# Kernel tuning notes

Hardware: AMD Instinct MI355X
Metric: run time of the kernel (lower is better)

Reference implementation:

```python
import jax, jax.numpy as jnp
import numpy as np

B, A, D, H, S, C, NB = 8192, 8, 4096, 1024, 32, 32, 8
BS = D // NB          # 512: hidden block size
IBS = (2 * H) // NB   # 256: input block size (gru input = action_embed ++ stoch_embed)
UNIMIX = 0.01


def setup_inputs() -> dict:
    key = jax.random.key(0)
    ks = jax.random.split(key, 16)
    rn = lambda k, shape, s=1.0: jax.random.normal(k, shape, jnp.float32) * s
    return {
        'deterministic': rn(ks[0], (B, D)),
        'stochastic': jax.random.uniform(ks[1], (B, S, C), jnp.float32),
        'prev_action': rn(ks[2], (B, A)),
        'embed': rn(ks[3], (B, H)),
        'is_first': jax.random.bernoulli(ks[4], 0.1, (B,)),
        # encoders (nn.Linear stores weight as [out, in])
        'W_act': rn(ks[5], (H, A), 1.0 / np.sqrt(A)), 'b_act': jnp.zeros((H,)),
        'W_stoch': rn(ks[6], (H, S * C), 1.0 / np.sqrt(S * C)), 'b_stoch': jnp.zeros((H,)),
        # block-diagonal GRU: per-block [3*BS, IBS] and [3*BS, BS]
        'W_ih': rn(ks[7], (NB, 3 * BS, IBS), 1.0 / np.sqrt(IBS)), 'b_ih': jnp.zeros((NB, 3 * BS)),
        'W_hh': rn(ks[8], (NB, 3 * BS, BS), 1.0 / np.sqrt(BS)), 'b_hh': jnp.zeros((NB, 3 * BS)),
        # prior net: D -> H -> S*C
        'W_pr1': rn(ks[9], (H, D), 1.0 / np.sqrt(D)), 'b_pr1': jnp.zeros((H,)),
        'W_pr2': rn(ks[10], (S * C, H), 1.0 / np.sqrt(H)), 'b_pr2': jnp.zeros((S * C,)),
        # posterior net: D+H -> H -> S*C
        'W_po1': rn(ks[11], (H, D + H), 1.0 / np.sqrt(D + H)), 'b_po1': jnp.zeros((H,)),
        'W_po2': rn(ks[12], (S * C, H), 1.0 / np.sqrt(H)), 'b_po2': jnp.zeros((S * C,)),
    }


def _forward(deterministic, stochastic, prev_action, embed, is_first,
             W_act, b_act, W_stoch, b_stoch, W_ih, b_ih, W_hh, b_hh,
             W_pr1, b_pr1, W_pr2, b_pr2, W_po1, b_po1, W_po2, b_po2):
    # reset state where is_first (initial_state is all zeros)
    det = jnp.where(is_first[:, None], 0.0, deterministic)
    stoch = jnp.where(is_first[:, None, None], 0.0, stochastic)
    # action normalization (magnitude detached)
    mag = jnp.maximum(jnp.max(jnp.abs(prev_action), axis=-1, keepdims=True), 1.0)
    act = prev_action / jax.lax.stop_gradient(mag)
    # encoders
    ae = act @ W_act.T + b_act                         # [B, H]
    se = stoch.reshape(stoch.shape[0], -1) @ W_stoch.T + b_stoch  # [B, H]
    x = jnp.concatenate([ae, se], axis=-1)             # [B, 2H]
    # block-diagonal GRU: batched small GEMMs over NB blocks
    xb = x.reshape(-1, NB, IBS)
    hb = det.reshape(-1, NB, BS)
    gates = (jnp.einsum('bki,koi->bko', xb, W_ih) + b_ih
             + jnp.einsum('bkj,koj->bko', hb, W_hh) + b_hh)  # [B, NB, 3*BS]
    gates = gates.reshape(-1, NB, 3, BS)
    reset = jax.nn.sigmoid(gates[:, :, 0])
    update = jax.nn.sigmoid(gates[:, :, 1])
    cand = jnp.tanh(reset * gates[:, :, 2])
    h_new = ((1.0 - update) * hb + update * cand).reshape(-1, D)  # [B, D]
    # prior head
    ph = jax.nn.silu(h_new @ W_pr1.T + b_pr1)
    prior_logits = ph @ W_pr2.T + b_pr2                # [B, S*C]
    pp = jax.nn.softmax(prior_logits.reshape(-1, S, C), axis=-1)
    prior_probs = ((1.0 - UNIMIX) * pp + UNIMIX / C).reshape(-1, S * C)
    # posterior head
    qh = jax.nn.silu(jnp.concatenate([h_new, embed], axis=-1) @ W_po1.T + b_po1)
    post_logits = qh @ W_po2.T + b_po2                 # [B, S*C]
    return jnp.concatenate([h_new, prior_logits, prior_probs, post_logits], axis=-1)


def reference(deterministic, stochastic, prev_action, embed, is_first,
              W_act, b_act, W_stoch, b_stoch, W_ih, b_ih, W_hh, b_hh,
              W_pr1, b_pr1, W_pr2, b_pr2, W_po1, b_po1, W_po2, b_po2):
    return _forward(deterministic, stochastic, prev_action, embed, is_first,
                    W_act, b_act, W_stoch, b_stoch, W_ih, b_ih, W_hh, b_hh,
                    W_pr1, b_pr1, W_pr2, b_pr2, W_po1, b_po1, W_po2, b_po2)
```

## Files before the change

kernel.cpp:

```cpp
#include <hip/hip_runtime.h>

typedef unsigned short u16;
typedef short bf16x8 __attribute__((ext_vector_type(8)));
typedef float f32x4 __attribute__((ext_vector_type(4)));

#define BSZ 8192
#define OUTLD 7168

__device__ __forceinline__ u16 f2bf(float f) {
  union { float f; unsigned u; } v; v.f = f;
  unsigned r = v.u + 0x7FFFu + ((v.u >> 16) & 1u);
  return (u16)(r >> 16);
}
__device__ __forceinline__ float bf2f(u16 h) {
  union { unsigned u; float f; } v; v.u = ((unsigned)h) << 16;
  return v.f;
}
__device__ __forceinline__ float sigmoidf_(float x) { return 1.0f / (1.0f + __expf(-x)); }
__device__ __forceinline__ float tanhf_(float t) { return 2.0f / (1.0f + __expf(-2.0f * t)) - 1.0f; }

__device__ __forceinline__ void gload16(const u16* g, u16* l) {
  __builtin_amdgcn_global_load_lds(
      (const __attribute__((address_space(1))) void*)g,
      (__attribute__((address_space(3))) void*)l, 16, 0, 0);
}

__global__ void k_detect(const unsigned* __restrict__ isf, int* __restrict__ flag) {
  __shared__ unsigned red;
  if (threadIdx.x == 0) red = 0u;
  __syncthreads();
  unsigned v = 0;
  for (int i = threadIdx.x; i < 2048; i += 256) v |= isf[i];
  atomicOr(&red, v);
  __syncthreads();
  if (threadIdx.x == 0)
    *flag = (((red & 0xFFFFFF00u) != 0u) && ((red & 0xFEFEFEFEu) == 0u)) ? 1 : 0;
}

__device__ __forceinline__ bool is_first_row(const void* isf, int fl, int b) {
  return fl ? (((const unsigned char*)isf)[b] != 0) : (((const int*)isf)[b] != 0);
}

struct Cv5 { const float* s[5]; u16* d[5]; long n4[5]; };
__global__ void k_cvtW(Cv5 c, long total4) {
  long stride = (long)gridDim.x * blockDim.x;
  for (long i = blockIdx.x * (long)blockDim.x + threadIdx.x; i < total4; i += stride) {
    long rem = i; int k = 0;
    while (k < 4 && rem >= c.n4[k]) { rem -= c.n4[k]; ++k; }
    float4 v = ((const float4*)c.s[k])[rem];
    ushort4 o; o.x = f2bf(v.x); o.y = f2bf(v.y); o.z = f2bf(v.z); o.w = f2bf(v.w);
    ((ushort4*)c.d[k])[rem] = o;
  }
}

__global__ void k_cvt_gruW(const float* __restrict__ sIh, u16* __restrict__ dIh,
                           const float* __restrict__ sHh, u16* __restrict__ dHh) {
  const long nIh = 393216L, total = 1179648L;
  long stride = (long)gridDim.x * blockDim.x;
  for (long i = blockIdx.x * (long)blockDim.x + threadIdx.x; i < total; i += stride) {
    const float* src; u16* dst; int ldk; long rel;
    if (i < nIh) { src = sIh; dst = dIh; ldk = 256; rel = i; }
    else         { src = sHh; dst = dHh; ldk = 512; rel = i - nIh; }
    int kc = ldk >> 3;
    int j = (int)(rel % kc); long row = rel / kc;
    long blk = row / 1536; int rP = (int)(row % 1536);
    int sHi = rP / 48, rem = rP % 48, g = rem >> 4, sLo = rem & 15;
    int srow = g * 512 + sHi * 16 + sLo;
    const float* s = src + (blk * 1536 + srow) * (long)ldk + j * 8;
    float4 v0 = ((const float4*)s)[0], v1 = ((const float4*)s)[1];
    ushort4 o0; o0.x = f2bf(v0.x); o0.y = f2bf(v0.y); o0.z = f2bf(v0.z); o0.w = f2bf(v0.w);
    ushort4 o1; o1.x = f2bf(v1.x); o1.y = f2bf(v1.y); o1.z = f2bf(v1.z); o1.w = f2bf(v1.w);
    ((ushort4*)(dst + rel * 8))[0] = o0;
    ((ushort4*)(dst + rel * 8))[1] = o1;
  }
}

struct Prep3 { const float* s[3]; u16* d[3]; long n4[3]; int c4[3]; int doR[3]; };
__global__ void k_prep(Prep3 p, const void* __restrict__ isf, const int* __restrict__ flag) {
  int fl = *flag;
  long stride = (long)gridDim.x * blockDim.x;
  long gid = blockIdx.x * (long)blockDim.x + threadIdx.x;
#pragma unroll 1
  for (int k = 0; k < 3; ++k) {
    const float4* src = (const float4*)p.s[k];
    ushort4* dst = (ushort4*)p.d[k];
    long n = p.n4[k]; int c4 = p.c4[k], doR = p.doR[k];
    for (long i = gid; i < n; i += stride) {
      float4 v = src[i];
      if (doR && is_first_row(isf, fl, (int)(i / c4))) { v.x = v.y = v.z = v.w = 0.f; }
      ushort4 o; o.x = f2bf(v.x); o.y = f2bf(v.y); o.z = f2bf(v.z); o.w = f2bf(v.w);
      dst[i] = o;
    }
  }
}

__global__ void k_ae(const float* __restrict__ act, const float* __restrict__ Wact,
                     const float* __restrict__ bact, u16* __restrict__ x) {
  long stride = (long)gridDim.x * blockDim.x;
  for (long t = blockIdx.x * (long)blockDim.x + threadIdx.x; t < (long)BSZ * 256; t += stride) {
    int b = (int)(t >> 8), h0 = (int)(t & 255) * 4;
    float4 a0 = ((const float4*)act)[b * 2];
    float4 a1 = ((const float4*)act)[b * 2 + 1];
    float mag = fmaxf(
        fmaxf(fmaxf(fabsf(a0.x), fabsf(a0.y)), fmaxf(fabsf(a0.z), fabsf(a0.w))),
        fmaxf(fmaxf(fabsf(a1.x), fabsf(a1.y)), fmaxf(fabsf(a1.z), fabsf(a1.w))));
    float inv = 1.0f / fmaxf(mag, 1.0f);
    ushort4 o;
    u16* op = (u16*)&o;
#pragma unroll
    for (int j = 0; j < 4; ++j) {
      int h = h0 + j;
      float4 w0 = ((const float4*)Wact)[h * 2];
      float4 w1 = ((const float4*)Wact)[h * 2 + 1];
      float dot = a0.x * w0.x + a0.y * w0.y + a0.z * w0.z + a0.w * w0.w
                + a1.x * w1.x + a1.y * w1.y + a1.z * w1.z + a1.w * w1.w;
      op[j] = f2bf(dot * inv + bact[h]);
    }
    *(ushort4*)&x[(long)b * 2048 + h0] = o;
  }
}

struct GDesc {
  const u16* A1; const u16* A2;
  int lda1, lda2, K1, K2;
  const u16* W1; const u16* W2;
  int ldw1, ldw2;
  const float* bias;
  float* outF; int ldoF;
  u16* outB; int ldoB;
  int actSilu;
};

__global__ __launch_bounds__(256, 3) void gemm128(GDesc d0, GDesc d1) {
  const GDesc d = blockIdx.z ? d1 : d0;
  __shared__ __align__(16) u16 lsA[128 * 64];
  __shared__ __align__(16) u16 lsB[128 * 64];
  const int tid = threadIdx.x;
  const int wave = tid >> 6, lane = tid & 63;
  const int m0 = blockIdx.x * 128, n0 = blockIdx.y * 128;
  const int wr = (wave >> 1) * 64, wc = (wave & 1) * 64;
  const int lrow = lane & 15;
  const int lq = lane >> 4;
  const int lr7 = lrow & 7;
  const int grow = wave * 8 + (lane >> 3);
  const int gcol = ((lane & 7) ^ (lane >> 3)) * 8;
  const int ro0 = ((lq ^ lr7)) * 8;
  const int ro1 = (((4 | lq) ^ lr7)) * 8;

  const f32x4 z4 = {0.f, 0.f, 0.f, 0.f};
  f32x4 acc[4][4];
#pragma unroll
  for (int m = 0; m < 4; ++m)
#pragma unroll
    for (int c = 0; c < 4; ++c) acc[m][c] = z4;

#pragma unroll 1
  for (int phse = 0; phse < 2; ++phse) {
    const u16* A = phse ? d.A2 : d.A1;
    const u16* W = phse ? d.W2 : d.W1;
    const int lda = phse ? d.lda2 : d.lda1;
    const int ldw = phse ? d.ldw2 : d.ldw1;
    const int K = phse ? d.K2 : d.K1;
#pragma unroll 1
    for (int k0 = 0; k0 < K; k0 += 64) {
      __syncthreads();
#pragma unroll
      for (int i = 0; i < 4; ++i) {
        gload16(&A[(long)(m0 + i * 32 + grow) * lda + k0 + gcol], &lsA[i * 2048 + wave * 512]);
        gload16(&W[(long)(n0 + i * 32 + grow) * ldw + k0 + gcol], &lsB[i * 2048 + wave * 512]);
      }
      __syncthreads();
#pragma unroll
      for (int kk = 0; kk < 2; ++kk) {
        const int ro = kk ? ro1 : ro0;
        bf16x8 af[4], wfr[4];
#pragma unroll
        for (int m = 0; m < 4; ++m)
          af[m] = *(const bf16x8*)&lsA[(wr + m * 16 + lrow) * 64 + ro];
#pragma unroll
        for (int c = 0; c < 4; ++c)
          wfr[c] = *(const bf16x8*)&lsB[(wc + c * 16 + lrow) * 64 + ro];
#pragma unroll
        for (int m = 0; m < 4; ++m)
#pragma unroll
          for (int c = 0; c < 4; ++c)
            acc[m][c] = __builtin_amdgcn_mfma_f32_16x16x32_bf16(af[m], wfr[c], acc[m][c], 0, 0, 0);
      }
    }
  }

#pragma unroll
  for (int c = 0; c < 4; ++c) {
    const int col = n0 + wc + c * 16 + lrow;
    const float bv = d.bias ? d.bias[col] : 0.f;
#pragma unroll
    for (int m = 0; m < 4; ++m) {
      const int rowb = m0 + wr + m * 16 + (lane >> 4) * 4;
#pragma unroll
      for (int r = 0; r < 4; ++r) {
        float v = acc[m][c][r] + bv;
        if (d.actSilu) v = v * sigmoidf_(v);
        if (d.outF) d.outF[(long)(rowb + r) * d.ldoF + col] = v;
        if (d.outB) d.outB[(long)(rowb + r) * d.ldoB + col] = f2bf(v);
      }
    }
  }
}

__global__ __launch_bounds__(256, 4) void gru96(
    const u16* __restrict__ xbuf, const u16* __restrict__ hbuf,
    const u16* __restrict__ WihP, const u16* __restrict__ WhhP,
    const float* __restrict__ bih, const float* __restrict__ bhh,
    float* __restrict__ outF, u16* __restrict__ hnew)
{
  __shared__ __align__(16) u16 lsA[128 * 64];
  __shared__ __align__(16) u16 lsW[96 * 64];
  const int tid = threadIdx.x;
  const int wave = tid >> 6, lane = tid & 63;
  const int wm = wave >> 1;
  const int wn = wave & 1;
  const int m0 = blockIdx.x * 128;
  const int blk = blockIdx.y >> 4;
  const int sp = blockIdx.y & 15;
  const int lrow = lane & 15;
  const int lq = lane >> 4;
  const int lr7 = lane & 7;
  const int gcol = ((lane & 7) ^ (lane >> 3)) * 8;
  const int ro0 = ((lq ^ lr7)) * 8;
  const int ro1 = (((4 | lq) ^ lr7)) * 8;

  const f32x4 z4 = {0.f, 0.f, 0.f, 0.f};
  f32x4 acc[4][3];
#pragma unroll
  for (int m = 0; m < 4; ++m)
#pragma unroll
    for (int g = 0; g < 3; ++g) acc[m][g] = z4;

#pragma unroll 1
  for (int phse = 0; phse < 2; ++phse) {
    const u16* A = phse ? (hbuf + blk * 512) : (xbuf + blk * 256);
    const u16* W = phse ? (WhhP + (long)blk * 786432 + sp * 49152)
                        : (WihP + (long)blk * 393216 + sp * 24576);
    const int lda = phse ? 4096 : 2048;
    const int ldw = phse ? 512 : 256;
    const int K = phse ? 512 : 256;
#pragma unroll 1
    for (int k0 = 0; k0 < K; k0 += 64) {
      __syncthreads();
#pragma unroll
      for (int r = 0; r < 4; ++r) {
        const int chunk = r * 4 + wave;
        gload16(&A[(long)(m0 + chunk * 8 + (lane >> 3)) * lda + k0 + gcol], &lsA[chunk * 512]);
      }
#pragma unroll
      for (int r = 0; r < 3; ++r) {
        const int chunk = r * 4 + wave;
        gload16(&W[(long)(chunk * 8 + (lane >> 3)) * ldw + k0 + gcol], &lsW[chunk * 512]);
      }
      __syncthreads();
#pragma unroll
      for (int kk = 0; kk < 2; ++kk) {
        const int ro = kk ? ro1 : ro0;
        bf16x8 af[4], wf[3];
#pragma unroll
        for (int m = 0; m < 4; ++m)
          af[m] = *(const bf16x8*)&lsA[(wm * 64 + m * 16 + lrow) * 64 + ro];
#pragma unroll
        for (int g = 0; g < 3; ++g)
          wf[g] = *(const bf16x8*)&lsW[(wn * 48 + g * 16 + lrow) * 64 + ro];
#pragma unroll
        for (int m = 0; m < 4; ++m)
#pragma unroll
          for (int g = 0; g < 3; ++g)
            acc[m][g] = __builtin_amdgcn_mfma_f32_16x16x32_bf16(af[m], wf[g], acc[m][g], 0, 0, 0);
      }
    }
  }

  const int s = sp * 32 + wn * 16 + lrow;
  const int col = blk * 512 + s;
  const long bb = (long)blk * 1536 + s;
  const float br = bih[bb] + bhh[bb];
  const float bu = bih[bb + 512] + bhh[bb + 512];
  const float bc = bih[bb + 1024] + bhh[bb + 1024];
#pragma unroll
  for (int m = 0; m < 4; ++m) {
    const int rowb = m0 + wm * 64 + m * 16 + lq * 4;
#pragma unroll
    for (int r = 0; r < 4; ++r) {
      const int row = rowb + r;
      const float gr = acc[m][0][r] + br;
      const float gu = acc[m][1][r] + bu;
      const float gc = acc[m][2][r] + bc;
      const float rr = sigmoidf_(gr);
      const float uu = sigmoidf_(gu);
      const float cand = tanhf_(rr * gc);
      const float h = bf2f(hbuf[(long)row * 4096 + col]);
      const float hn = (1.f - uu) * h + uu * cand;
      outF[(long)row * OUTLD + col] = hn;
      hnew[(long)row * 4096 + col] = f2bf(hn);
    }
  }
}

__global__ void k_softmax(float* __restrict__ out) {
  int t = blockIdx.x * blockDim.x + threadIdx.x;
  if (t >= BSZ * 32) return;
  int b = t >> 5, g = t & 31;
  const float* src = out + (long)b * OUTLD + 4096 + g * 32;
  float* dst = out + (long)b * OUTLD + 5120 + g * 32;
  float v[32];
#pragma unroll
  for (int i = 0; i < 8; ++i) {
    float4 q = ((const float4*)src)[i];
    v[4 * i] = q.x; v[4 * i + 1] = q.y; v[4 * i + 2] = q.z; v[4 * i + 3] = q.w;
  }
  float m = v[0];
#pragma unroll
  for (int i = 1; i < 32; ++i) m = fmaxf(m, v[i]);
  float ssum = 0.f;
#pragma unroll
  for (int i = 0; i < 32; ++i) { v[i] = __expf(v[i] - m); ssum += v[i]; }
  float inv = 0.99f / ssum;
#pragma unroll
  for (int i = 0; i < 8; ++i) {
    float4 q;
    q.x = v[4 * i] * inv + 3.125e-4f;
    q.y = v[4 * i + 1] * inv + 3.125e-4f;
    q.z = v[4 * i + 2] * inv + 3.125e-4f;
    q.w = v[4 * i + 3] * inv + 3.125e-4f;
    ((float4*)dst)[i] = q;
  }
}

extern "C" void kernel_launch(void* const* d_in, const int* in_sizes, int n_in,
                              void* d_out, int out_size, void* d_ws, size_t ws_size,
                              hipStream_t stream) {
  const float* det   = (const float*)d_in[0];
  const float* stoch = (const float*)d_in[1];
  const float* pact  = (const float*)d_in[2];
  const float* embed = (const float*)d_in[3];
  const void*  isf   = d_in[4];
  const float* Wact  = (const float*)d_in[5];
  const float* bact  = (const float*)d_in[6];
  const float* Wst   = (const float*)d_in[7];
  const float* bst   = (const float*)d_in[8];
  const float* Wih   = (const float*)d_in[9];
  const float* bih   = (const float*)d_in[10];
  const float* Whh   = (const float*)d_in[11];
  const float* bhh   = (const float*)d_in[12];
  const float* Wpr1  = (const float*)d_in[13];
  const float* bpr1  = (const float*)d_in[14];
  const float* Wpr2  = (const float*)d_in[15];
  const float* bpr2  = (const float*)d_in[16];
  const float* Wpo1  = (const float*)d_in[17];
  const float* bpo1  = (const float*)d_in[18];
  const float* Wpo2  = (const float*)d_in[19];
  const float* bpo2  = (const float*)d_in[20];
  float* out = (float*)d_out;

  int* flag = (int*)d_ws;
  u16* wsu  = (u16*)((char*)d_ws + 256);
  u16* bWst  = wsu;
  u16* bWihP = wsu + 1048576UL;
  u16* bWhhP = wsu + 4194304UL;
  u16* bWpr1 = wsu + 10485760UL;
  u16* bWpr2 = wsu + 14680064UL;
  u16* bWpo1 = wsu + 15728640UL;
  u16* bWpo2 = wsu + 20971520UL;
  u16* bufX  = wsu + 22020096UL;
  u16* bufSt = wsu + 38797312UL;
  u16* bufHb = wsu + 47185920UL;
  u16* bufHn = wsu + 80740352UL;
  u16* bufEm = wsu + 114294784UL;

  k_detect<<<dim3(1), dim3(256), 0, stream>>>((const unsigned*)isf, flag);

  Cv5 cw;
  cw.s[0] = Wst;  cw.d[0] = bWst;  cw.n4[0] = 262144L;
  cw.s[1] = Wpr1; cw.d[1] = bWpr1; cw.n4[1] = 1048576L;
  cw.s[2] = Wpr2; cw.d[2] = bWpr2; cw.n4[2] = 262144L;
  cw.s[3] = Wpo1; cw.d[3] = bWpo1; cw.n4[3] = 1310720L;
  cw.s[4] = Wpo2; cw.d[4] = bWpo2; cw.n4[4] = 262144L;
  k_cvtW<<<dim3(2048), dim3(256), 0, stream>>>(cw, 3145728L);

  k_cvt_gruW<<<dim3(2048), dim3(256), 0, stream>>>(Wih, bWihP, Whh, bWhhP);

  Prep3 pp;
  pp.s[0] = stoch; pp.d[0] = bufSt; pp.n4[0] = 2097152L; pp.c4[0] = 256;  pp.doR[0] = 1;
  pp.s[1] = det;   pp.d[1] = bufHb; pp.n4[1] = 8388608L; pp.c4[1] = 1024; pp.doR[1] = 1;
  pp.s[2] = embed; pp.d[2] = bufEm; pp.n4[2] = 2097152L; pp.c4[2] = 256;  pp.doR[2] = 0;
  k_prep<<<dim3(4096), dim3(256), 0, stream>>>(pp, isf, flag);

  k_ae<<<dim3(2048), dim3(256), 0, stream>>>(pact, Wact, bact, bufX);

  GDesc dSe;
  dSe.A1 = bufSt; dSe.A2 = nullptr; dSe.lda1 = 1024; dSe.lda2 = 0;
  dSe.K1 = 1024; dSe.K2 = 0;
  dSe.W1 = bWst; dSe.W2 = nullptr; dSe.ldw1 = 1024; dSe.ldw2 = 0;
  dSe.bias = bst; dSe.outF = nullptr; dSe.ldoF = 0;
  dSe.outB = bufX + 1024; dSe.ldoB = 2048; dSe.actSilu = 0;
  gemm128<<<dim3(64, 8, 1), dim3(256), 0, stream>>>(dSe, dSe);

  gru96<<<dim3(64, 128), dim3(256), 0, stream>>>(bufX, bufHb, bWihP, bWhhP,
                                                 bih, bhh, out, bufHn);

  GDesc dPr1, dPo1;
  dPr1.A1 = bufHn; dPr1.A2 = nullptr; dPr1.lda1 = 4096; dPr1.lda2 = 0;
  dPr1.K1 = 4096; dPr1.K2 = 0;
  dPr1.W1 = bWpr1; dPr1.W2 = nullptr; dPr1.ldw1 = 4096; dPr1.ldw2 = 0;
  dPr1.bias = bpr1; dPr1.outF = nullptr; dPr1.ldoF = 0;
  dPr1.outB = bufSt; dPr1.ldoB = 1024; dPr1.actSilu = 1;
  dPo1.A1 = bufHn; dPo1.A2 = bufEm; dPo1.lda1 = 4096; dPo1.lda2 = 1024;
  dPo1.K1 = 4096; dPo1.K2 = 1024;
  dPo1.W1 = bWpo1; dPo1.W2 = bWpo1 + 4096; dPo1.ldw1 = 5120; dPo1.ldw2 = 5120;
  dPo1.bias = bpo1; dPo1.outF = nullptr; dPo1.ldoF = 0;
  dPo1.outB = bufHb; dPo1.ldoB = 1024; dPo1.actSilu = 1;
  gemm128<<<dim3(64, 8, 2), dim3(256), 0, stream>>>(dPr1, dPo1);

  GDesc dPr2, dPo2;
  dPr2.A1 = bufSt; dPr2.A2 = nullptr; dPr2.lda1 = 1024; dPr2.lda2 = 0;
  dPr2.K1 = 1024; dPr2.K2 = 0;
  dPr2.W1 = bWpr2; dPr2.W2 = nullptr; dPr2.ldw1 = 1024; dPr2.ldw2 = 0;
  dPr2.bias = bpr2; dPr2.outF = out + 4096; dPr2.ldoF = OUTLD;
  dPr2.outB = nullptr; dPr2.ldoB = 0; dPr2.actSilu = 0;
  dPo2.A1 = bufHb; dPo2.A2 = nullptr; dPo2.lda1 = 1024; dPo2.lda2 = 0;
  dPo2.K1 = 1024; dPo2.K2 = 0;
  dPo2.W1 = bWpo2; dPo2.W2 = nullptr; dPo2.ldw1 = 1024; dPo2.ldw2 = 0;
  dPo2.bias = bpo2; dPo2.outF = out + 6144; dPo2.ldoF = OUTLD;
  dPo2.outB = nullptr; dPo2.ldoB = 0; dPo2.actSilu = 0;
  gemm128<<<dim3(64, 8, 2), dim3(256), 0, stream>>>(dPr2, dPo2);

  k_softmax<<<dim3(1024), dim3(256), 0, stream>>>(out);
}
```

Baseline: 670.2 us.

## Fuse preprocessing kernels into one launch and widen GRU tile to 192 columns

```diff
diff --git a/kernel.cpp b/kernel.cpp
--- a/kernel.cpp
+++ b/kernel.cpp
@@ -25,98 +25,91 @@
       (__attribute__((address_space(3))) void*)l, 16, 0, 0);
 }
 
-__global__ void k_detect(const unsigned* __restrict__ isf, int* __restrict__ flag) {
-  __shared__ unsigned red;
-  if (threadIdx.x == 0) red = 0u;
+struct FuseArgs {
+  const float* cs[5]; u16* cd[5]; long cn[5];
+  const float* sIh; u16* dIh; const float* sHh; u16* dHh;
+  const float* ps[3]; u16* pd[3]; long pn[3]; int pc4[3]; int pdoR[3];
+  const float* act; const float* Wact; const float* bact; u16* xout;
+  const void* isf;
+};
+
+__global__ void k_fuse(FuseArgs a) {
+  __shared__ unsigned redS;
+  if (threadIdx.x == 0) redS = 0u;
   __syncthreads();
-  unsigned v = 0;
-  for (int i = threadIdx.x; i < 2048; i += 256) v |= isf[i];
-  atomicOr(&red, v);
+  {
+    unsigned v = 0;
+    const unsigned* w = (const unsigned*)a.isf;
+    for (int i = threadIdx.x; i < 2048; i += 256) v |= w[i];
+    atomicOr(&redS, v);
+  }
   __syncthreads();
-  if (threadIdx.x == 0)
-    *flag = (((red & 0xFFFFFF00u) != 0u) && ((red & 0xFEFEFEFEu) == 0u)) ? 1 : 0;
-}
-
-__device__ __forceinline__ bool is_first_row(const void* isf, int fl, int b) {
-  return fl ? (((const unsigned char*)isf)[b] != 0) : (((const int*)isf)[b] != 0);
-}
-
-struct Cv5 { const float* s[5]; u16* d[5]; long n4[5]; };
-__global__ void k_cvtW(Cv5 c, long total4) {
+  const int fl = (((redS & 0xFFFFFF00u) != 0u) && ((redS & 0xFEFEFEFEu) == 0u)) ? 1 : 0;
+
+  const long B0 = 3145728L;
+  const long B1 = B0 + 1179648L;
+  const long B2 = B1 + 12582912L;
+  const long B3 = B2 + 2097152L;
+  const long nIh = 393216L;
+
   long stride = (long)gridDim.x * blockDim.x;
-  for (long i = blockIdx.x * (long)blockDim.x + threadIdx.x; i < total4; i += stride) {
-    long rem = i; int k = 0;
-    while (k < 4 && rem >= c.n4[k]) { rem -= c.n4[k]; ++k; }
-    float4 v = ((const float4*)c.s[k])[rem];
-    ushort4 o; o.x = f2bf(v.x); o.y = f2bf(v.y); o.z = f2bf(v.z); o.w = f2bf(v.w);
-    ((ushort4*)c.d[k])[rem] = o;
-  }
-}
-
-__global__ void k_cvt_gruW(const float* __restrict__ sIh, u16* __restrict__ dIh,
-                           const float* __restrict__ sHh, u16* __restrict__ dHh) {
-  const long nIh = 393216L, total = 1179648L;
-  long stride = (long)gridDim.x * blockDim.x;
-  for (long i = blockIdx.x * (long)blockDim.x + threadIdx.x; i < total; i += stride) {
-    const float* src; u16* dst; int ldk; long rel;
-    if (i < nIh) { src = sIh; dst = dIh; ldk = 256; rel = i; }
-    else         { src = sHh; dst = dHh; ldk = 512; rel = i - nIh; }
-    int kc = ldk >> 3;
-    int j = (int)(rel % kc); long row = rel / kc;
-    long blk = row / 1536; int rP = (int)(row % 1536);
-    int sHi = rP / 48, rem = rP % 48, g = rem >> 4, sLo = rem & 15;
-    int srow = g * 512 + sHi * 16 + sLo;
-    const float* s = src + (blk * 1536 + srow) * (long)ldk + j * 8;
-    float4 v0 = ((const float4*)s)[0], v1 = ((const float4*)s)[1];
-    ushort4 o0; o0.x = f2bf(v0.x); o0.y = f2bf(v0.y); o0.z = f2bf(v0.z); o0.w = f2bf(v0.w);
-    ushort4 o1; o1.x = f2bf(v1.x); o1.y = f2bf(v1.y); o1.z = f2bf(v1.z); o1.w = f2bf(v1.w);
-    ((ushort4*)(dst + rel * 8))[0] = o0;
-    ((ushort4*)(dst + rel * 8))[1] = o1;
-  }
-}
-
-struct Prep3 { const float* s[3]; u16* d[3]; long n4[3]; int c4[3]; int doR[3]; };
-__global__ void k_prep(Prep3 p, const void* __restrict__ isf, const int* __restrict__ flag) {
-  int fl = *flag;
-  long stride = (long)gridDim.x * blockDim.x;
-  long gid = blockIdx.x * (long)blockDim.x + threadIdx.x;
-#pragma unroll 1
-  for (int k = 0; k < 3; ++k) {
-    const float4* src = (const float4*)p.s[k];
-    ushort4* dst = (ushort4*)p.d[k];
-    long n = p.n4[k]; int c4 = p.c4[k], doR = p.doR[k];
-    for (long i = gid; i < n; i += stride) {
-      float4 v = src[i];
-      if (doR && is_first_row(isf, fl, (int)(i / c4))) { v.x = v.y = v.z = v.w = 0.f; }
+  for (long i = blockIdx.x * (long)blockDim.x + threadIdx.x; i < B3; i += stride) {
+    if (i < B0) {
+      long rem = i; int k = 0;
+      while (k < 4 && rem >= a.cn[k]) { rem -= a.cn[k]; ++k; }
+      float4 v = ((const float4*)a.cs[k])[rem];
       ushort4 o; o.x = f2bf(v.x); o.y = f2bf(v.y); o.z = f2bf(v.z); o.w = f2bf(v.w);
-      dst[i] = o;
+      ((ushort4*)a.cd[k])[rem] = o;
+    } else if (i < B1) {
+      long rel = i - B0;
+      const float* src; u16* dst; int ldk;
+      if (rel < nIh) { src = a.sIh; dst = a.dIh; ldk = 256; }
+      else           { src = a.sHh; dst = a.dHh; ldk = 512; rel -= nIh; }
+      int kc = ldk >> 3;
+      int j = (int)(rel % kc); long row = rel / kc;
+      long blk = row / 1536; int rP = (int)(row % 1536);
+      int sHi = rP / 48, rem = rP % 48, g = rem >> 4, sLo = rem & 15;
+      int srow = g * 512 + sHi * 16 + sLo;
+      const float* s = src + (blk * 1536 + srow) * (long)ldk + j * 8;
+      float4 v0 = ((const float4*)s)[0], v1 = ((const float4*)s)[1];
+      ushort4 o0; o0.x = f2bf(v0.x); o0.y = f2bf(v0.y); o0.z = f2bf(v0.z); o0.w = f2bf(v0.w);
+      ushort4 o1; o1.x = f2bf(v1.x); o1.y = f2bf(v1.y); o1.z = f2bf(v1.z); o1.w = f2bf(v1.w);
+      ((ushort4*)(dst + rel * 8))[0] = o0;
+      ((ushort4*)(dst + rel * 8))[1] = o1;
+    } else if (i < B2) {
+      long rel = i - B1; int k = 0;
+      while (k < 2 && rel >= a.pn[k]) { rel -= a.pn[k]; ++k; }
+      float4 v = ((const float4*)a.ps[k])[rel];
+      if (a.pdoR[k]) {
+        int b = (int)(rel / a.pc4[k]);
+        bool isf1 = fl ? (((const unsigned char*)a.isf)[b] != 0)
+                       : (((const int*)a.isf)[b] != 0);
+        if (isf1) { v.x = v.y = v.z = v.w = 0.f; }
+      }
+      ushort4 o; o.x = f2bf(v.x); o.y = f2bf(v.y); o.z = f2bf(v.z); o.w = f2bf(v.w);
+      ((ushort4*)a.pd[k])[rel] = o;
+    } else {
+      long t = i - B2;
+      int b = (int)(t >> 8), h0 = (int)(t & 255) * 4;
+      float4 a0 = ((const float4*)a.act)[b * 2];
+      float4 a1 = ((const float4*)a.act)[b * 2 + 1];
+      float mag = fmaxf(
+          fmaxf(fmaxf(fabsf(a0.x), fabsf(a0.y)), fmaxf(fabsf(a0.z), fabsf(a0.w))),
+          fmaxf(fmaxf(fabsf(a1.x), fabsf(a1.y)), fmaxf(fabsf(a1.z), fabsf(a1.w))));
+      float inv = 1.0f / fmaxf(mag, 1.0f);
+      ushort4 o;
+      u16* op = (u16*)&o;
+#pragma unroll
+      for (int j = 0; j < 4; ++j) {
+        int h = h0 + j;
+        float4 w0 = ((const float4*)a.Wact)[h * 2];
+        float4 w1 = ((const float4*)a.Wact)[h * 2 + 1];
+        float dot = a0.x * w0.x + a0.y * w0.y + a0.z * w0.z + a0.w * w0.w
+                  + a1.x * w1.x + a1.y * w1.y + a1.z * w1.z + a1.w * w1.w;
+        op[j] = f2bf(dot * inv + a.bact[h]);
+      }
+      *(ushort4*)&a.xout[(long)b * 2048 + h0] = o;
     }
-  }
-}
-
-__global__ void k_ae(const float* __restrict__ act, const float* __restrict__ Wact,
-                     const float* __restrict__ bact, u16* __restrict__ x) {
-  long stride = (long)gridDim.x * blockDim.x;
-  for (long t = blockIdx.x * (long)blockDim.x + threadIdx.x; t < (long)BSZ * 256; t += stride) {
-    int b = (int)(t >> 8), h0 = (int)(t & 255) * 4;
-    float4 a0 = ((const float4*)act)[b * 2];
-    float4 a1 = ((const float4*)act)[b * 2 + 1];
-    float mag = fmaxf(
-        fmaxf(fmaxf(fabsf(a0.x), fabsf(a0.y)), fmaxf(fabsf(a0.z), fabsf(a0.w))),
-        fmaxf(fmaxf(fabsf(a1.x), fabsf(a1.y)), fmaxf(fabsf(a1.z), fabsf(a1.w))));
-    float inv = 1.0f / fmaxf(mag, 1.0f);
-    ushort4 o;
-    u16* op = (u16*)&o;
-#pragma unroll
-    for (int j = 0; j < 4; ++j) {
-      int h = h0 + j;
-      float4 w0 = ((const float4*)Wact)[h * 2];
-      float4 w1 = ((const float4*)Wact)[h * 2 + 1];
-      float dot = a0.x * w0.x + a0.y * w0.y + a0.z * w0.z + a0.w * w0.w
-                + a1.x * w1.x + a1.y * w1.y + a1.z * w1.z + a1.w * w1.w;
-      op[j] = f2bf(dot * inv + bact[h]);
-    }
-    *(ushort4*)&x[(long)b * 2048 + h0] = o;
   }
 }
 
@@ -207,21 +200,21 @@
   }
 }
 
-__global__ __launch_bounds__(256, 4) void gru96(
+__global__ __launch_bounds__(256, 3) void gru192(
     const u16* __restrict__ xbuf, const u16* __restrict__ hbuf,
     const u16* __restrict__ WihP, const u16* __restrict__ WhhP,
     const float* __restrict__ bih, const float* __restrict__ bhh,
     float* __restrict__ outF, u16* __restrict__ hnew)
 {
   __shared__ __align__(16) u16 lsA[128 * 64];
-  __shared__ __align__(16) u16 lsW[96 * 64];
+  __shared__ __align__(16) u16 lsW[192 * 64];
   const int tid = threadIdx.x;
   const int wave = tid >> 6, lane = tid & 63;
   const int wm = wave >> 1;
   const int wn = wave & 1;
   const int m0 = blockIdx.x * 128;
-  const int blk = blockIdx.y >> 4;
-  const int sp = blockIdx.y & 15;
+  const int blk = blockIdx.y >> 3;
+  const int sp = blockIdx.y & 7;
   const int lrow = lane & 15;
   const int lq = lane >> 4;
   const int lr7 = lane & 7;
@@ -230,17 +223,19 @@
   const int ro1 = (((4 | lq) ^ lr7)) * 8;
 
   const f32x4 z4 = {0.f, 0.f, 0.f, 0.f};
-  f32x4 acc[4][3];
+  f32x4 acc[4][2][3];
 #pragma unroll
   for (int m = 0; m < 4; ++m)
 #pragma unroll
-    for (int g = 0; g < 3; ++g) acc[m][g] = z4;
+    for (int sg = 0; sg < 2; ++sg)
+#pragma unroll
+      for (int g = 0; g < 3; ++g) acc[m][sg][g] = z4;
 
 #pragma unroll 1
   for (int phse = 0; phse < 2; ++phse) {
     const u16* A = phse ? (hbuf + blk * 512) : (xbuf + blk * 256);
-    const u16* W = phse ? (WhhP + (long)blk * 786432 + sp * 49152)
-                        : (WihP + (long)blk * 393216 + sp * 24576);
+    const u16* W = phse ? (WhhP + (long)blk * 786432 + sp * 98304)
+                        : (WihP + (long)blk * 393216 + sp * 49152);
     const int lda = phse ? 4096 : 2048;
     const int ldw = phse ? 512 : 256;
     const int K = phse ? 512 : 256;
@@ -253,7 +248,7 @@
         gload16(&A[(long)(m0 + chunk * 8 + (lane >> 3)) * lda + k0 + gcol], &lsA[chunk * 512]);
       }
 #pragma unroll
-      for (int r = 0; r < 3; ++r) {
+      for (int r = 0; r < 6; ++r) {
         const int chunk = r * 4 + wave;
         gload16(&W[(long)(chunk * 8 + (lane >> 3)) * ldw + k0 + gcol], &lsW[chunk * 512]);
       }
@@ -261,44 +256,51 @@
 #pragma unroll
       for (int kk = 0; kk < 2; ++kk) {
         const int ro = kk ? ro1 : ro0;
-        bf16x8 af[4], wf[3];
+        bf16x8 af[4], wf[2][3];
 #pragma unroll
         for (int m = 0; m < 4; ++m)
           af[m] = *(const bf16x8*)&lsA[(wm * 64 + m * 16 + lrow) * 64 + ro];
 #pragma unroll
-        for (int g = 0; g < 3; ++g)
-          wf[g] = *(const bf16x8*)&lsW[(wn * 48 + g * 16 + lrow) * 64 + ro];
+        for (int sg = 0; sg < 2; ++sg)
+#pragma unroll
+          for (int g = 0; g < 3; ++g)
+            wf[sg][g] = *(const bf16x8*)&lsW[(wn * 96 + sg * 48 + g * 16 + lrow) * 64 + ro];
 #pragma unroll
         for (int m = 0; m < 4; ++m)
 #pragma unroll
-          for (int g = 0; g < 3; ++g)
-            acc[m][g] = __builtin_amdgcn_mfma_f32_16x16x32_bf16(af[m], wf[g], acc[m][g], 0, 0, 0);
+          for (int sg = 0; sg < 2; ++sg)
+#pragma unroll
+            for (int g = 0; g < 3; ++g)
+              acc[m][sg][g] = __builtin_amdgcn_mfma_f32_16x16x32_bf16(af[m], wf[sg][g], acc[m][sg][g], 0, 0, 0);
       }
     }
   }
 
-  const int s = sp * 32 + wn * 16 + lrow;
-  const int col = blk * 512 + s;
-  const long bb = (long)blk * 1536 + s;
-  const float br = bih[bb] + bhh[bb];
-  const float bu = bih[bb + 512] + bhh[bb + 512];
-  const float bc = bih[bb + 1024] + bhh[bb + 1024];
-#pragma unroll
-  for (int m = 0; m < 4; ++m) {
-    const int rowb = m0 + wm * 64 + m * 16 + lq * 4;
-#pragma unroll
-    for (int r = 0; r < 4; ++r) {
-      const int row = rowb + r;
-      const float gr = acc[m][0][r] + br;
-      const float gu = acc[m][1][r] + bu;
-      const float gc = acc[m][2][r] + bc;
-      const float rr = sigmoidf_(gr);
-      const float uu = sigmoidf_(gu);
-      const float cand = tanhf_(rr * gc);
-      const float h = bf2f(hbuf[(long)row * 4096 + col]);
-      const float hn = (1.f - uu) * h + uu * cand;
-      outF[(long)row * OUTLD + col] = hn;
-      hnew[(long)row * 4096 + col] = f2bf(hn);
+#pragma unroll
+  for (int sg = 0; sg < 2; ++sg) {
+    const int s = sp * 64 + wn * 32 + sg * 16 + lrow;
+    const int col = blk * 512 + s;
+    const long bb = (long)blk * 1536 + s;
+    const float br = bih[bb] + bhh[bb];
+    const float bu = bih[bb + 512] + bhh[bb + 512];
+    const float bc = bih[bb + 1024] + bhh[bb + 1024];
+#pragma unroll
+    for (int m = 0; m < 4; ++m) {
+      const int rowb = m0 + wm * 64 + m * 16 + lq * 4;
+#pragma unroll
+      for (int r = 0; r < 4; ++r) {
+        const int row = rowb + r;
+        const float gr = acc[m][sg][0][r] + br;
+        const float gu = acc[m][sg][1][r] + bu;
+        const float gc = acc[m][sg][2][r] + bc;
+        const float rr = sigmoidf_(gr);
+        const float uu = sigmoidf_(gu);
+        const float cand = tanhf_(rr * gc);
+        const float h = bf2f(hbuf[(long)row * 4096 + col]);
+        const float hn = (1.f - uu) * h + uu * cand;
+        outF[(long)row * OUTLD + col] = hn;
+        hnew[(long)row * 4096 + col] = f2bf(hn);
+      }
     }
   }
 }
@@ -359,7 +361,6 @@
   const float* bpo2  = (const float*)d_in[20];
   float* out = (float*)d_out;
 
-  int* flag = (int*)d_ws;
   u16* wsu  = (u16*)((char*)d_ws + 256);
   u16* bWst  = wsu;
   u16* bWihP = wsu + 1048576UL;
@@ -374,25 +375,19 @@
   u16* bufHn = wsu + 80740352UL;
   u16* bufEm = wsu + 114294784UL;
 
-  k_detect<<<dim3(1), dim3(256), 0, stream>>>((const unsigned*)isf, flag);
-
-  Cv5 cw;
-  cw.s[0] = Wst;  cw.d[0] = bWst;  cw.n4[0] = 262144L;
-  cw.s[1] = Wpr1; cw.d[1] = bWpr1; cw.n4[1] = 1048576L;
-  cw.s[2] = Wpr2; cw.d[2] = bWpr2; cw.n4[2] = 262144L;
-  cw.s[3] = Wpo1; cw.d[3] = bWpo1; cw.n4[3] = 1310720L;
-  cw.s[4] = Wpo2; cw.d[4] = bWpo2; cw.n4[4] = 262144L;
-  k_cvtW<<<dim3(2048), dim3(256), 0, stream>>>(cw, 3145728L);
-
-  k_cvt_gruW<<<dim3(2048), dim3(256), 0, stream>>>(Wih, bWihP, Whh, bWhhP);
-
-  Prep3 pp;
-  pp.s[0] = stoch; pp.d[0] = bufSt; pp.n4[0] = 2097152L; pp.c4[0] = 256;  pp.doR[0] = 1;
-  pp.s[1] = det;   pp.d[1] = bufHb; pp.n4[1] = 8388608L; pp.c4[1] = 1024; pp.doR[1] = 1;
-  pp.s[2] = embed; pp.d[2] = bufEm; pp.n4[2] = 2097152L; pp.c4[2] = 256;  pp.doR[2] = 0;
-  k_prep<<<dim3(4096), dim3(256), 0, stream>>>(pp, isf, flag);
-
-  k_ae<<<dim3(2048), dim3(256), 0, stream>>>(pact, Wact, bact, bufX);
+  FuseArgs fa;
+  fa.cs[0] = Wst;  fa.cd[0] = bWst;  fa.cn[0] = 262144L;
+  fa.cs[1] = Wpr1; fa.cd[1] = bWpr1; fa.cn[1] = 1048576L;
+  fa.cs[2] = Wpr2; fa.cd[2] = bWpr2; fa.cn[2] = 262144L;
+  fa.cs[3] = Wpo1; fa.cd[3] = bWpo1; fa.cn[3] = 1310720L;
+  fa.cs[4] = Wpo2; fa.cd[4] = bWpo2; fa.cn[4] = 262144L;
+  fa.sIh = Wih; fa.dIh = bWihP; fa.sHh = Whh; fa.dHh = bWhhP;
+  fa.ps[0] = stoch; fa.pd[0] = bufSt; fa.pn[0] = 2097152L; fa.pc4[0] = 256;  fa.pdoR[0] = 1;
+  fa.ps[1] = det;   fa.pd[1] = bufHb; fa.pn[1] = 8388608L; fa.pc4[1] = 1024; fa.pdoR[1] = 1;
+  fa.ps[2] = embed; fa.pd[2] = bufEm; fa.pn[2] = 2097152L; fa.pc4[2] = 256;  fa.pdoR[2] = 0;
+  fa.act = pact; fa.Wact = Wact; fa.bact = bact; fa.xout = bufX;
+  fa.isf = isf;
+  k_fuse<<<dim3(4096), dim3(256), 0, stream>>>(fa);
 
   GDesc dSe;
   dSe.A1 = bufSt; dSe.A2 = nullptr; dSe.lda1 = 1024; dSe.lda2 = 0;
@@ -402,7 +397,7 @@
   dSe.outB = bufX + 1024; dSe.ldoB = 2048; dSe.actSilu = 0;
   gemm128<<<dim3(64, 8, 1), dim3(256), 0, stream>>>(dSe, dSe);
 
-  gru96<<<dim3(64, 128), dim3(256), 0, stream>>>(bufX, bufHb, bWihP, bWhhP,
+  gru192<<<dim3(64, 64), dim3(256), 0, stream>>>(bufX, bufHb, bWihP, bWhhP,
                                                  bih, bhh, out, bufHn);
 
   GDesc dPr1, dPo1;
```

After: 702.4 us. +4.8%, slower.
